# Kernel tuning notes

Hardware: AMD Instinct MI355X
Metric: run time of the kernel (lower is better)

The kernel has to match this reference:

```python
import jax, jax.numpy as jnp
import numpy as np

B, N, D, F = 4, 4096, 1024, 64
LN_EPS = 1e-5
ATTN_EPS = 1e-6


def setup_inputs() -> dict:
    key = jax.random.key(0)
    ks = jax.random.split(key, 9)
    s = 0.02  # small init scale for weights
    return {
        "x": jax.random.normal(ks[0], (B, N, D), dtype=jnp.float32),
        "ln1_w": jnp.ones((D,), jnp.float32),
        "ln1_b": jnp.zeros((D,), jnp.float32),
        "q_w": jax.random.normal(ks[1], (F, D), jnp.float32) * s,
        "q_b": jnp.zeros((F,), jnp.float32),
        "k_w": jax.random.normal(ks[2], (F, D), jnp.float32) * s,
        "k_b": jnp.zeros((F,), jnp.float32),
        "v_w": jax.random.normal(ks[3], (D, D), jnp.float32) * s,
        "v_b": jnp.zeros((D,), jnp.float32),
        "o_w": jax.random.normal(ks[4], (D, D), jnp.float32) * s,
        "o_b": jnp.zeros((D,), jnp.float32),
        "ln2_w": jnp.ones((D,), jnp.float32),
        "ln2_b": jnp.zeros((D,), jnp.float32),
        "f1_w": jax.random.normal(ks[5], (4 * D, D), jnp.float32) * s,
        "f1_b": jnp.zeros((4 * D,), jnp.float32),
        "f2_w": jax.random.normal(ks[6], (D, 4 * D), jnp.float32) * s,
        "f2_b": jnp.zeros((D,), jnp.float32),
    }


def _layer_norm(x, w, b):
    mu = jnp.mean(x, axis=-1, keepdims=True)
    var = jnp.var(x, axis=-1, keepdims=True)
    return (x - mu) * jax.lax.rsqrt(var + LN_EPS) * w + b


def _linear(x, w, b):
    # torch nn.Linear convention: y = x @ w.T + b, w: [out, in]
    return jnp.einsum('bnd,fd->bnf', x, w) + b


def _causal_linear_attn(Q, K, V, eps=ATTN_EPS):
    """Q,K: [B,N,F] positive features; V: [B,N,D]. Recurrent causal scan."""
    b, n, f = K.shape
    d = V.shape[-1]
    Qt = jnp.swapaxes(Q, 0, 1)  # [N,B,F]
    Kt = jnp.swapaxes(K, 0, 1)
    Vt = jnp.swapaxes(V, 0, 1)  # [N,B,D]

    def step(carry, qkv):
        KV, Ks = carry  # [B,F,D], [B,F]
        q, k, v = qkv
        KV = KV + k[:, :, None] * v[:, None, :]
        Ks = Ks + k
        num = jnp.einsum('bf,bfd->bd', q, KV)
        den = jnp.sum(q * Ks, axis=-1, keepdims=True) + eps
        return (KV, Ks), num / den

    init = (jnp.zeros((b, f, d), Q.dtype), jnp.zeros((b, f), Q.dtype))
    _, out = jax.lax.scan(step, init, (Qt, Kt, Vt))
    return jnp.swapaxes(out, 0, 1)  # [B,N,D]


def reference(x, ln1_w, ln1_b, q_w, q_b, k_w, k_b, v_w, v_b,
              o_w, o_b, ln2_w, ln2_b, f1_w, f1_b, f2_w, f2_b):
    x_norm = _layer_norm(x, ln1_w, ln1_b)
    # LinearHopfieldASA, causal=True
    Q = jax.nn.elu(_linear(x_norm, q_w, q_b)) + 1.0  # positive feature map
    K = jax.nn.elu(_linear(x_norm, k_w, k_b)) + 1.0
    V = _linear(x_norm, v_w, v_b)
    attn = _causal_linear_attn(Q, K, V)
    attn = _linear(attn, o_w, o_b)
    x = x + attn
    h = _layer_norm(x, ln2_w, ln2_b)
    h = jax.nn.gelu(_linear(h, f1_w, f1_b), approximate=False)
    x = x + _linear(h, f2_w, f2_b)
    return x
```

## Files before the change

kernel.cpp:

```cpp
#include <hip/hip_runtime.h>
#include <hip/hip_bf16.h>
#include <cstdint>
#include <cstddef>


typedef __attribute__((ext_vector_type(8))) short short8;
typedef __attribute__((ext_vector_type(4))) short short4v;
typedef __attribute__((ext_vector_type(4))) float floatx4;
typedef __attribute__((ext_vector_type(4))) unsigned short ushort4v;

#define DEV static __device__ __forceinline__

DEV float b2f(unsigned short u) {
    union { unsigned int i; float f; } v; v.i = ((unsigned int)u) << 16; return v.f;
}
DEV unsigned short f2b(float f) {
    union { float f; unsigned int i; } v; v.f = f;
    unsigned int i = v.i;
    unsigned int r = (i + 0x7FFFu + ((i >> 16) & 1u)) >> 16;
    return (unsigned short)r;
}

DEV void gl_lds16(const void* g, void* l) {
    __builtin_amdgcn_global_load_lds((const __attribute__((address_space(1))) void*)g,
                                     (__attribute__((address_space(3))) void*)l, 16, 0, 0);
}

__global__ void eel_prep(const float* __restrict__ qw, const float* __restrict__ kw,
                         const float* __restrict__ vw, const float* __restrict__ ow,
                         const float* __restrict__ f1w, const float* __restrict__ f2w,
                         const float* __restrict__ qb, const float* __restrict__ kb,
                         const float* __restrict__ vb,
                         uint16_t* __restrict__ Wqkv, uint16_t* __restrict__ Wo,
                         uint16_t* __restrict__ W1, uint16_t* __restrict__ W2,
                         float* __restrict__ bqkv)
{
    size_t i = (size_t)blockIdx.x * 256 + threadIdx.x;
    size_t stride = (size_t)gridDim.x * 256;
    for (size_t t = i; t < 1152u * 1024u; t += stride) {
        int r = (int)(t >> 10);
        float v = (r < 64) ? qw[t] : (r < 128) ? kw[t - 65536] : vw[t - 131072];
        Wqkv[t] = f2b(v);
    }
    for (size_t t = i; t < 1048576u; t += stride) Wo[t] = f2b(ow[t]);
    for (size_t t = i; t < 4194304u; t += stride) { W1[t] = f2b(f1w[t]); W2[t] = f2b(f2w[t]); }
    if (i < 1152) bqkv[i] = (i < 64) ? qb[i] : (i < 128) ? kb[i - 64] : vb[i - 128];
}

__global__ __launch_bounds__(256) void eel_ln(const float* __restrict__ x,
                                              const float* __restrict__ w,
                                              const float* __restrict__ b,
                                              uint16_t* __restrict__ out)
{
    int row = blockIdx.x, tid = threadIdx.x;
    float4 xv = ((const float4*)(x + (size_t)row * 1024))[tid];
    float s  = xv.x + xv.y + xv.z + xv.w;
    float s2 = xv.x*xv.x + xv.y*xv.y + xv.z*xv.z + xv.w*xv.w;
#pragma unroll
    for (int off = 32; off > 0; off >>= 1) {
        s  += __shfl_down(s, off);
        s2 += __shfl_down(s2, off);
    }
    __shared__ float ps[8];
    int wv = tid >> 6;
    if ((tid & 63) == 0) { ps[wv] = s; ps[4 + wv] = s2; }
    __syncthreads();
    float mu  = (ps[0] + ps[1] + ps[2] + ps[3]) * (1.0f / 1024.0f);
    float var = (ps[4] + ps[5] + ps[6] + ps[7]) * (1.0f / 1024.0f) - mu * mu;
    float rs = rsqrtf(var + 1e-5f);
    float4 wv4 = ((const float4*)w)[tid];
    float4 bv4 = ((const float4*)b)[tid];
    ushort4v o;
    o.x = f2b((xv.x - mu) * rs * wv4.x + bv4.x);
    o.y = f2b((xv.y - mu) * rs * wv4.y + bv4.y);
    o.z = f2b((xv.z - mu) * rs * wv4.z + bv4.z);
    o.w = f2b((xv.w - mu) * rs * wv4.w + bv4.w);
    *(ushort4v*)(out + (size_t)row * 1024 + tid * 4) = o;
}

#define BM 128
#define BN 128
#define BKK 64

__global__ __launch_bounds__(256, 2) void eel_gemm(
    const uint16_t* __restrict__ A, int lda,
    const uint16_t* __restrict__ Bm, int ldb,
    int K,
    const float* __restrict__ bias,
    const float* __restrict__ res,
    uint16_t* __restrict__ outb,
    float* __restrict__ outf,
    int ldc, int mode)
{
    __shared__ uint16_t As[BM * BKK];
    __shared__ uint16_t Bs[BN * BKK];
    int tid = threadIdx.x;
    int lane = tid & 63, w = tid >> 6;
    int lin  = blockIdx.y * gridDim.x + blockIdx.x;
    int span = 8 * gridDim.y;
    int g = lin / span, r = lin % span;
    int bx = g * 8 + (r & 7);
    int by = r >> 3;
    int m0 = bx * BM, n0 = by * BN;
    int wr = (w >> 1) * 64, wc = (w & 1) * 64;
    int quad = lane >> 4, l16 = lane & 15;
    floatx4 acc[4][4] = {};

    int nkb = K / BKK;
    for (int kb = 0; kb < nkb; ++kb) {
        int k0 = kb * BKK;
#pragma unroll
        for (int it = 0; it < 4; ++it) {
            int seg = it * 256 + tid;
            int row = seg >> 3, sub = seg & 7;
            int gs = sub ^ (row & 7);
            gl_lds16(A + (size_t)(m0 + row) * lda + k0 + gs * 8, (char*)As + seg * 16);
            gl_lds16(Bm + (size_t)(n0 + row) * ldb + k0 + gs * 8, (char*)Bs + seg * 16);
        }
        __syncthreads();
#pragma unroll
        for (int ks = 0; ks < 2; ++ks) {
            short8 a[4], b[4];
#pragma unroll
            for (int i = 0; i < 4; i++) {
                int mrow = wr + i * 16 + l16;
                int sa = (ks * 4 + quad) ^ (mrow & 7);
                a[i] = *(const short8*)((const char*)As + mrow * (BKK * 2) + sa * 16);
                int nrow = wc + i * 16 + l16;
                int sb = (ks * 4 + quad) ^ (nrow & 7);
                b[i] = *(const short8*)((const char*)Bs + nrow * (BKK * 2) + sb * 16);
            }
#pragma unroll
            for (int i = 0; i < 4; i++)
#pragma unroll
                for (int j = 0; j < 4; j++)
                    acc[i][j] = __builtin_amdgcn_mfma_f32_16x16x32_bf16(a[i], b[j], acc[i][j], 0, 0, 0);
        }
        __syncthreads();
    }

#pragma unroll
    for (int j = 0; j < 4; j++) {
        int col = n0 + wc + j * 16 + l16;
        float bv = bias ? bias[col] : 0.0f;
#pragma unroll
        for (int i = 0; i < 4; i++) {
#pragma unroll
            for (int r2 = 0; r2 < 4; r2++) {
                int row = m0 + wr + i * 16 + quad * 4 + r2;
                float v = acc[i][j][r2] + bv;
                size_t off = (size_t)row * ldc + col;
                if (mode == 0) {
                    if (col < 128) v = (v > 0.f) ? v + 1.f : __expf(v);
                    outb[off] = f2b(v);
                } else if (mode == 1) {
                    outf[off] = v + res[off];
                } else {
                    float u = 0.7978845608028654f * v * (1.0f + 0.044715f * v * v);
                    float e = __expf(2.0f * u);
                    float t = 1.0f - 2.0f / (e + 1.0f);
                    v = 0.5f * v * (1.0f + t);
                    outb[off] = f2b(v);
                }
            }
        }
    }
}

__global__ __launch_bounds__(256) void eel_attn_s(
    const uint16_t* __restrict__ QKV,
    uint16_t* __restrict__ Sg,
    float* __restrict__ den,
    float* __restrict__ KsA)
{
    int chunk = blockIdx.x, tid = threadIdx.x;
    int tok0 = chunk * 64;
    __shared__ uint16_t Q[64 * 64];
    __shared__ uint16_t Kc[64 * 64];
    __shared__ float denp[64][4];
    {
        int nloc = tid >> 2, seg = tid & 3;
        const uint16_t* src = QKV + (size_t)(tok0 + nloc) * 1152 + seg * 16;
        *(short8*)(Q + nloc * 64 + seg * 16)     = *(const short8*)(src);
        *(short8*)(Q + nloc * 64 + seg * 16 + 8) = *(const short8*)(src + 8);
        src += 64;
        *(short8*)(Kc + nloc * 64 + seg * 16)     = *(const short8*)(src);
        *(short8*)(Kc + nloc * 64 + seg * 16 + 8) = *(const short8*)(src + 8);
    }
    __syncthreads();
    if (tid < 64) {
        float s = 0.f;
        for (int m = 0; m < 64; m++) s += b2f(Kc[m * 64 + tid]);
        KsA[chunk * 64 + tid] = s;
    }
    int n = tid >> 2, mg = tid & 3;
    float dsum = 0.f;
    for (int mi = 0; mi < 16; mi++) {
        int m = mg * 16 + mi;
        size_t soff = (size_t)(tok0 + n) * 64 + m;
        if (m <= n) {
            float s = 0.f;
#pragma unroll
            for (int f = 0; f < 64; f += 8) {
                short8 q8 = *(const short8*)(Q + n * 64 + f);
                short8 k8 = *(const short8*)(Kc + m * 64 + f);
#pragma unroll
                for (int j = 0; j < 8; j++)
                    s += b2f((unsigned short)q8[j]) * b2f((unsigned short)k8[j]);
            }
            dsum += s;
            Sg[soff] = f2b(s);
        } else {
            Sg[soff] = 0;
        }
    }
    denp[n][mg] = dsum;
    __syncthreads();
    if (tid < 64)
        den[tok0 + tid] = denp[tid][0] + denp[tid][1] + denp[tid][2] + denp[tid][3];
}

__global__ __launch_bounds__(256) void eel_attn_kv(
    const uint16_t* __restrict__ QKV,
    uint16_t* __restrict__ KV_A)
{
    int bi = blockIdx.x;
    int chunk = bi >> 3, p = bi & 7;
    int tid = threadIdx.x;
    int tok0 = chunk * 64;
    __shared__ uint16_t Kc[64 * 64];
    __shared__ uint16_t Vp[64 * 128];
    {
        int r = tid >> 2, sg = tid & 3;
        const uint16_t* src = QKV + (size_t)(tok0 + r) * 1152 + 64 + sg * 16;
        *(short8*)(Kc + r * 64 + sg * 16)     = *(const short8*)(src);
        *(short8*)(Kc + r * 64 + sg * 16 + 8) = *(const short8*)(src + 8);
    }
#pragma unroll
    for (int it = 0; it < 2; it++) {
        int s = it * 256 + tid;
        int r = s >> 3, sub = s & 7;
        const uint16_t* src = QKV + (size_t)(tok0 + r) * 1152 + 128 + p * 128 + sub * 16;
        *(short8*)(Vp + r * 128 + sub * 16)     = *(const short8*)(src);
        *(short8*)(Vp + r * 128 + sub * 16 + 8) = *(const short8*)(src + 8);
    }
    __syncthreads();
    int f0 = (tid >> 5) * 8, d0 = (tid & 31) * 4;
    float acc[8][4] = {};
#pragma unroll 2
    for (int m = 0; m < 64; m++) {
        short8 k8 = *(const short8*)(Kc + m * 64 + f0);
        short4v v4 = *(const short4v*)(Vp + m * 128 + d0);
        float v0 = b2f((unsigned short)v4[0]), v1 = b2f((unsigned short)v4[1]);
        float v2 = b2f((unsigned short)v4[2]), v3 = b2f((unsigned short)v4[3]);
#pragma unroll
        for (int i = 0; i < 8; i++) {
            float kk = b2f((unsigned short)k8[i]);
            acc[i][0] += kk * v0; acc[i][1] += kk * v1;
            acc[i][2] += kk * v2; acc[i][3] += kk * v3;
        }
    }
#pragma unroll
    for (int i = 0; i < 8; i++) {
        ushort4v st;
        st.x = f2b(acc[i][0]); st.y = f2b(acc[i][1]);
        st.z = f2b(acc[i][2]); st.w = f2b(acc[i][3]);
        *(ushort4v*)(KV_A + ((size_t)chunk * 64 + f0 + i) * 1024 + p * 128 + d0) = st;
    }
}

__global__ __launch_bounds__(256) void eel_kv_prefix(
    const uint16_t* __restrict__ KV_A, uint16_t* __restrict__ KV_P)
{
    int bi = blockIdx.x;
    int b = bi >> 8, rem = bi & 255;
    int f = rem >> 2;
    int d = (rem & 3) * 256 + threadIdx.x;
    float acc = 0.f;
    for (int cc = 0; cc < 64; cc++) {
        size_t idx = (((size_t)(b * 64 + cc)) * 64 + f) * 1024 + d;
        KV_P[idx] = f2b(acc);
        acc += b2f(KV_A[idx]);
    }
}

__global__ void eel_ks_prefix(const float* __restrict__ KsA, float* __restrict__ KsP)
{
    int b = blockIdx.x, f = threadIdx.x;
    float acc = 0.f;
    for (int cc = 0; cc < 64; cc++) {
        int idx = (b * 64 + cc) * 64 + f;
        KsP[idx] = acc;
        acc += KsA[idx];
    }
}

__global__ __launch_bounds__(256) void eel_attn_out(
    const uint16_t* __restrict__ QKV,
    const uint16_t* __restrict__ Sg,
    const float* __restrict__ den,
    const float* __restrict__ KsP,
    const uint16_t* __restrict__ KV_P,
    uint16_t* __restrict__ attn)
{
    int bi = blockIdx.x;
    int chunk = bi >> 3, p = bi & 7;
    int tid = threadIdx.x;
    int tok0 = chunk * 64;
    __shared__ uint16_t Qt[64 * 64];
    __shared__ uint16_t St[64 * 64];
    __shared__ uint16_t Vp[64 * 128];
    __shared__ uint16_t KVp[64 * 128];
    __shared__ float dfull[64];
    {
        int n = tid >> 2, fs = (tid & 3) * 16;
        const uint16_t* qsrc = QKV + (size_t)(tok0 + n) * 1152 + fs;
        short8 a0 = *(const short8*)(qsrc);
        short8 a1 = *(const short8*)(qsrc + 8);
        const uint16_t* ssrc = Sg + (size_t)(tok0 + n) * 64 + fs;
        short8 s0 = *(const short8*)(ssrc);
        short8 s1 = *(const short8*)(ssrc + 8);
#pragma unroll
        for (int j = 0; j < 8; j++) {
            Qt[(fs + j) * 64 + n]     = (unsigned short)a0[j];
            Qt[(fs + 8 + j) * 64 + n] = (unsigned short)a1[j];
            St[(fs + j) * 64 + n]     = (unsigned short)s0[j];
            St[(fs + 8 + j) * 64 + n] = (unsigned short)s1[j];
        }
    }
#pragma unroll
    for (int it = 0; it < 2; it++) {
        int s = it * 256 + tid;
        int r = s >> 3, sub = s & 7;
        const uint16_t* vsrc = QKV + (size_t)(tok0 + r) * 1152 + 128 + p * 128 + sub * 16;
        *(short8*)(Vp + r * 128 + sub * 16)     = *(const short8*)(vsrc);
        *(short8*)(Vp + r * 128 + sub * 16 + 8) = *(const short8*)(vsrc + 8);
        const uint16_t* kvsrc = KV_P + ((size_t)(chunk * 64 + r)) * 1024 + p * 128 + sub * 16;
        *(short8*)(KVp + r * 128 + sub * 16)     = *(const short8*)(kvsrc);
        *(short8*)(KVp + r * 128 + sub * 16 + 8) = *(const short8*)(kvsrc + 8);
    }
    __syncthreads();
    if (tid < 64) {
        float s = 0.f;
        for (int f = 0; f < 64; f++)
            s += b2f(Qt[f * 64 + tid]) * KsP[chunk * 64 + f];
        dfull[tid] = s + den[tok0 + tid] + 1e-6f;
    }
    __syncthreads();
    int n0 = (tid >> 5) * 8, d0 = (tid & 31) * 4;
    float acc[8][4] = {};
#pragma unroll 2
    for (int f = 0; f < 64; f++) {
        short8 q8 = *(const short8*)(Qt + f * 64 + n0);
        short4v kv4 = *(const short4v*)(KVp + f * 128 + d0);
        float v0 = b2f((unsigned short)kv4[0]), v1 = b2f((unsigned short)kv4[1]);
        float v2 = b2f((unsigned short)kv4[2]), v3 = b2f((unsigned short)kv4[3]);
#pragma unroll
        for (int i = 0; i < 8; i++) {
            float q = b2f((unsigned short)q8[i]);
            acc[i][0] += q * v0; acc[i][1] += q * v1;
            acc[i][2] += q * v2; acc[i][3] += q * v3;
        }
    }
#pragma unroll 2
    for (int m = 0; m < 64; m++) {
        short8 s8 = *(const short8*)(St + m * 64 + n0);
        short4v v4 = *(const short4v*)(Vp + m * 128 + d0);
        float v0 = b2f((unsigned short)v4[0]), v1 = b2f((unsigned short)v4[1]);
        float v2 = b2f((unsigned short)v4[2]), v3 = b2f((unsigned short)v4[3]);
#pragma unroll
        for (int i = 0; i < 8; i++) {
            float q = b2f((unsigned short)s8[i]);
            acc[i][0] += q * v0; acc[i][1] += q * v1;
            acc[i][2] += q * v2; acc[i][3] += q * v3;
        }
    }
#pragma unroll
    for (int i = 0; i < 8; i++) {
        int n = n0 + i;
        float rinv = 1.0f / dfull[n];
        ushort4v st;
        st.x = f2b(acc[i][0] * rinv);
        st.y = f2b(acc[i][1] * rinv);
        st.z = f2b(acc[i][2] * rinv);
        st.w = f2b(acc[i][3] * rinv);
        *(ushort4v*)(attn + (size_t)(tok0 + n) * 1024 + p * 128 + d0) = st;
    }
}

extern "C" void kernel_launch(void* const* d_in, const int* in_sizes, int n_in,
                              void* d_out, int out_size, void* d_ws, size_t ws_size,
                              hipStream_t stream)
{
    (void)in_sizes; (void)n_in; (void)out_size; (void)ws_size;
    const float* x     = (const float*)d_in[0];
    const float* ln1w  = (const float*)d_in[1];
    const float* ln1b  = (const float*)d_in[2];
    const float* qw    = (const float*)d_in[3];
    const float* qb    = (const float*)d_in[4];
    const float* kw    = (const float*)d_in[5];
    const float* kb    = (const float*)d_in[6];
    const float* vw    = (const float*)d_in[7];
    const float* vb    = (const float*)d_in[8];
    const float* ow    = (const float*)d_in[9];
    const float* ob    = (const float*)d_in[10];
    const float* ln2w  = (const float*)d_in[11];
    const float* ln2b  = (const float*)d_in[12];
    const float* f1w   = (const float*)d_in[13];
    const float* f1b   = (const float*)d_in[14];
    const float* f2w   = (const float*)d_in[15];
    const float* f2bs  = (const float*)d_in[16];
    float* out = (float*)d_out;
    char* ws = (char*)d_ws;

    const size_t o_Wqkv = 0;
    const size_t o_Wo   = o_Wqkv + 2359296;
    const size_t o_W1   = o_Wo   + 2097152;
    const size_t o_W2   = o_W1   + 8388608;
    const size_t o_bqkv = o_W2   + 8388608;
    const size_t O_XN   = 21238272;
    const size_t O_QKV  = 54792704;
    const size_t O_S    = 92541440;
    const size_t O_DEN  = 94638592;
    const size_t O_KSA  = 94704128;
    const size_t O_KSP  = 94769664;
    const size_t O_KVA  = 94835200;
    const size_t O_KVP  = 161944064;

    uint16_t* Wqkv  = (uint16_t*)(ws + o_Wqkv);
    uint16_t* Wo    = (uint16_t*)(ws + o_Wo);
    uint16_t* W1    = (uint16_t*)(ws + o_W1);
    uint16_t* W2    = (uint16_t*)(ws + o_W2);
    float*    bqkv  = (float*)(ws + o_bqkv);
    uint16_t* xn    = (uint16_t*)(ws + O_XN);
    uint16_t* attn  = (uint16_t*)(ws + O_XN);
    uint16_t* QKV   = (uint16_t*)(ws + O_QKV);
    uint16_t* hnorm = (uint16_t*)(ws + O_QKV);
    uint16_t* Sg    = (uint16_t*)(ws + O_S);
    float*    den   = (float*)(ws + O_DEN);
    float*    KsA   = (float*)(ws + O_KSA);
    float*    KsP   = (float*)(ws + O_KSP);
    uint16_t* KV_A  = (uint16_t*)(ws + O_KVA);
    uint16_t* hbuf  = (uint16_t*)(ws + O_KVA);
    uint16_t* KV_P  = (uint16_t*)(ws + O_KVP);

    eel_prep<<<4096, 256, 0, stream>>>(qw, kw, vw, ow, f1w, f2w, qb, kb, vb,
                                       Wqkv, Wo, W1, W2, bqkv);
    eel_ln<<<16384, 256, 0, stream>>>(x, ln1w, ln1b, xn);
    eel_gemm<<<dim3(128, 9), 256, 0, stream>>>(xn, 1024, Wqkv, 1024, 1024,
                                               bqkv, nullptr, QKV, nullptr, 1152, 0);
    eel_attn_s<<<256, 256, 0, stream>>>(QKV, Sg, den, KsA);
    eel_attn_kv<<<2048, 256, 0, stream>>>(QKV, KV_A);
    eel_kv_prefix<<<1024, 256, 0, stream>>>(KV_A, KV_P);
    eel_ks_prefix<<<4, 64, 0, stream>>>(KsA, KsP);
    eel_attn_out<<<2048, 256, 0, stream>>>(QKV, Sg, den, KsP, KV_P, attn);
    eel_gemm<<<dim3(128, 8), 256, 0, stream>>>(attn, 1024, Wo, 1024, 1024,
                                               ob, x, nullptr, out, 1024, 1);
    eel_ln<<<16384, 256, 0, stream>>>(out, ln2w, ln2b, hnorm);
    for (int strip = 0; strip < 2; strip++) {
        size_t noff = (size_t)strip * 2048;
        eel_gemm<<<dim3(128, 16), 256, 0, stream>>>(hnorm, 1024, W1 + noff * 1024, 1024, 1024,
                                                    f1b + noff, nullptr, hbuf, nullptr, 2048, 2);
        eel_gemm<<<dim3(128, 8), 256, 0, stream>>>(hbuf, 2048, W2 + noff, 4096, 2048,
                                                   strip == 0 ? f2bs : nullptr, out, nullptr,
                                                   out, 1024, 1);
    }
}
```

Baseline: 857.8 us.

## Replace GEMM with 256x256-tile, 4-stage pipelined 8-wave kernel

Replaces the 128x128 single-buffered GEMM with a 256x256-tile kernel using 512 threads, a 4-deep LDS ring of BK=32 stages filled by direct global-to-LDS loads, explicit vmcnt waits, split-phase MFMA with setprio, and a new XOR swizzle. It also changes the tile rasterization and adds bounds clamping for the 1152-wide QKV output. The aim is to overlap global loads with MFMA work and raise data reuse per block. In exchange it uses more LDS and registers (32 accumulators per wave) and launches fewer blocks, which can leave CUs underused on the smaller GEMMs.

```diff
diff --git a/kernel.cpp b/kernel.cpp
--- a/kernel.cpp
+++ b/kernel.cpp
@@ -78,93 +78,162 @@
     *(ushort4v*)(out + (size_t)row * 1024 + tid * 4) = o;
 }
 
-#define BM 128
-#define BN 128
-#define BKK 64
-
-__global__ __launch_bounds__(256, 2) void eel_gemm(
+__global__ __launch_bounds__(512, 2) void eel_gemm256(
     const uint16_t* __restrict__ A, int lda,
-    const uint16_t* __restrict__ Bm, int ldb,
+    const uint16_t* __restrict__ Bm, int ldb, int bmax,
     int K,
     const float* __restrict__ bias,
     const float* __restrict__ res,
-    uint16_t* __restrict__ outb,
-    float* __restrict__ outf,
-    int ldc, int mode)
-{
-    __shared__ uint16_t As[BM * BKK];
-    __shared__ uint16_t Bs[BN * BKK];
+    uint16_t* __restrict__ outb, float* __restrict__ outf,
+    int ldc, int mode, int nvalid)
+{
+    __shared__ uint16_t sA[4][8192];
+    __shared__ uint16_t sB[4][8192];
     int tid = threadIdx.x;
     int lane = tid & 63, w = tid >> 6;
-    int lin  = blockIdx.y * gridDim.x + blockIdx.x;
-    int span = 8 * gridDim.y;
-    int g = lin / span, r = lin % span;
-    int bx = g * 8 + (r & 7);
-    int by = r >> 3;
-    int m0 = bx * BM, n0 = by * BN;
-    int wr = (w >> 1) * 64, wc = (w & 1) * 64;
     int quad = lane >> 4, l16 = lane & 15;
-    floatx4 acc[4][4] = {};
-
-    int nkb = K / BKK;
-    for (int kb = 0; kb < nkb; ++kb) {
-        int k0 = kb * BKK;
-#pragma unroll
-        for (int it = 0; it < 4; ++it) {
-            int seg = it * 256 + tid;
-            int row = seg >> 3, sub = seg & 7;
-            int gs = sub ^ (row & 7);
-            gl_lds16(A + (size_t)(m0 + row) * lda + k0 + gs * 8, (char*)As + seg * 16);
-            gl_lds16(Bm + (size_t)(n0 + row) * ldb + k0 + gs * 8, (char*)Bs + seg * 16);
-        }
-        __syncthreads();
-#pragma unroll
-        for (int ks = 0; ks < 2; ++ks) {
-            short8 a[4], b[4];
-#pragma unroll
-            for (int i = 0; i < 4; i++) {
-                int mrow = wr + i * 16 + l16;
-                int sa = (ks * 4 + quad) ^ (mrow & 7);
-                a[i] = *(const short8*)((const char*)As + mrow * (BKK * 2) + sa * 16);
-                int nrow = wc + i * 16 + l16;
-                int sb = (ks * 4 + quad) ^ (nrow & 7);
-                b[i] = *(const short8*)((const char*)Bs + nrow * (BKK * 2) + sb * 16);
-            }
-#pragma unroll
-            for (int i = 0; i < 4; i++)
-#pragma unroll
-                for (int j = 0; j < 4; j++)
-                    acc[i][j] = __builtin_amdgcn_mfma_f32_16x16x32_bf16(a[i], b[j], acc[i][j], 0, 0, 0);
-        }
-        __syncthreads();
-    }
+
+    int nblk = gridDim.x, qch = nblk >> 3;
+    int lin  = blockIdx.x;
+    int tile = (lin & 7) * qch + (lin >> 3);
+    int bx = tile & 63, by = tile >> 6;
+    int m0 = bx << 8, n0 = by << 8;
+
+    int wr = (w >> 2) * 128;
+    int wc = (w & 3) * 64;
+    int rA = wr + l16;
+    int rB = wc + l16;
+
+    floatx4 acc[8][4] = {};
+    short8 a0, a1, a2, a3, b0, b1, b2, b3;
+
+    int srow = tid >> 2, sseg = tid & 3;
+    int sgs  = sseg ^ ((srow >> 1) & 3);
+    const uint16_t* aptr0 = A + (size_t)(m0 + srow) * lda + sgs * 8;
+    const uint16_t* aptr1 = A + (size_t)(m0 + srow + 128) * lda + sgs * 8;
+    int br0 = n0 + srow;       if (br0 >= bmax) br0 = 0;
+    int br1 = n0 + srow + 128; if (br1 >= bmax) br1 = 0;
+    const uint16_t* bptr0 = Bm + (size_t)br0 * ldb + sgs * 8;
+    const uint16_t* bptr1 = Bm + (size_t)br1 * ldb + sgs * 8;
+
+#define STAGE_A(Tn) do {                                                      \
+    gl_lds16(aptr0 + (Tn) * 32, (char*)sA[(Tn) & 3] + tid * 16);              \
+    gl_lds16(aptr1 + (Tn) * 32, (char*)sA[(Tn) & 3] + 8192 + tid * 16);       \
+} while (0)
+#define STAGE_B(Tn) do {                                                      \
+    gl_lds16(bptr0 + (Tn) * 32, (char*)sB[(Tn) & 3] + tid * 16);              \
+    gl_lds16(bptr1 + (Tn) * 32, (char*)sB[(Tn) & 3] + 8192 + tid * 16);       \
+} while (0)
+#define NOSTG do { } while (0)
+#define FRG(buf, r) (*(const short8*)((const char*)(buf) + (size_t)(r) * 64 + \
+                     ((quad ^ (((r) >> 1) & 3)) * 16)))
+#define VMW8 do { asm volatile("s_waitcnt vmcnt(8)"); __builtin_amdgcn_sched_barrier(0); } while (0)
+#define VMW4 do { asm volatile("s_waitcnt vmcnt(4)"); __builtin_amdgcn_sched_barrier(0); } while (0)
+#define VMW0 do { asm volatile("s_waitcnt vmcnt(0)"); __builtin_amdgcn_sched_barrier(0); } while (0)
+#define MFMA16(bb) do {                                                                        \
+    acc[(bb)+0][0]=__builtin_amdgcn_mfma_f32_16x16x32_bf16(a0,b0,acc[(bb)+0][0],0,0,0);        \
+    acc[(bb)+0][1]=__builtin_amdgcn_mfma_f32_16x16x32_bf16(a0,b1,acc[(bb)+0][1],0,0,0);        \
+    acc[(bb)+0][2]=__builtin_amdgcn_mfma_f32_16x16x32_bf16(a0,b2,acc[(bb)+0][2],0,0,0);        \
+    acc[(bb)+0][3]=__builtin_amdgcn_mfma_f32_16x16x32_bf16(a0,b3,acc[(bb)+0][3],0,0,0);        \
+    acc[(bb)+1][0]=__builtin_amdgcn_mfma_f32_16x16x32_bf16(a1,b0,acc[(bb)+1][0],0,0,0);        \
+    acc[(bb)+1][1]=__builtin_amdgcn_mfma_f32_16x16x32_bf16(a1,b1,acc[(bb)+1][1],0,0,0);        \
+    acc[(bb)+1][2]=__builtin_amdgcn_mfma_f32_16x16x32_bf16(a1,b2,acc[(bb)+1][2],0,0,0);        \
+    acc[(bb)+1][3]=__builtin_amdgcn_mfma_f32_16x16x32_bf16(a1,b3,acc[(bb)+1][3],0,0,0);        \
+    acc[(bb)+2][0]=__builtin_amdgcn_mfma_f32_16x16x32_bf16(a2,b0,acc[(bb)+2][0],0,0,0);        \
+    acc[(bb)+2][1]=__builtin_amdgcn_mfma_f32_16x16x32_bf16(a2,b1,acc[(bb)+2][1],0,0,0);        \
+    acc[(bb)+2][2]=__builtin_amdgcn_mfma_f32_16x16x32_bf16(a2,b2,acc[(bb)+2][2],0,0,0);        \
+    acc[(bb)+2][3]=__builtin_amdgcn_mfma_f32_16x16x32_bf16(a2,b3,acc[(bb)+2][3],0,0,0);        \
+    acc[(bb)+3][0]=__builtin_amdgcn_mfma_f32_16x16x32_bf16(a3,b0,acc[(bb)+3][0],0,0,0);        \
+    acc[(bb)+3][1]=__builtin_amdgcn_mfma_f32_16x16x32_bf16(a3,b1,acc[(bb)+3][1],0,0,0);        \
+    acc[(bb)+3][2]=__builtin_amdgcn_mfma_f32_16x16x32_bf16(a3,b2,acc[(bb)+3][2],0,0,0);        \
+    acc[(bb)+3][3]=__builtin_amdgcn_mfma_f32_16x16x32_bf16(a3,b3,acc[(bb)+3][3],0,0,0);        \
+} while (0)
+#define PHASE1(bi, STG) do {                                                  \
+    const uint16_t* Ab_ = sA[bi]; const uint16_t* Bb_ = sB[bi];               \
+    a0 = FRG(Ab_, rA +  0); a1 = FRG(Ab_, rA + 16);                           \
+    a2 = FRG(Ab_, rA + 32); a3 = FRG(Ab_, rA + 48);                           \
+    b0 = FRG(Bb_, rB +  0); b1 = FRG(Bb_, rB + 16);                           \
+    b2 = FRG(Bb_, rB + 32); b3 = FRG(Bb_, rB + 48);                           \
+    STG;                                                                      \
+    __builtin_amdgcn_s_barrier();                                             \
+    asm volatile("s_waitcnt lgkmcnt(0)");                                     \
+    __builtin_amdgcn_sched_barrier(0);                                        \
+    __builtin_amdgcn_s_setprio(1);                                            \
+    MFMA16(0);                                                                \
+    __builtin_amdgcn_s_setprio(0);                                            \
+    __builtin_amdgcn_s_barrier();                                             \
+} while (0)
+#define PHASE2(bi, STG, VM) do {                                              \
+    const uint16_t* Ab_ = sA[bi];                                             \
+    a0 = FRG(Ab_, rA + 64); a1 = FRG(Ab_, rA + 80);                           \
+    a2 = FRG(Ab_, rA + 96); a3 = FRG(Ab_, rA + 112);                          \
+    STG;                                                                      \
+    __builtin_amdgcn_s_barrier();                                             \
+    asm volatile("s_waitcnt lgkmcnt(0)");                                     \
+    __builtin_amdgcn_sched_barrier(0);                                        \
+    __builtin_amdgcn_s_setprio(1);                                            \
+    MFMA16(4);                                                                \
+    __builtin_amdgcn_s_setprio(0);                                            \
+    VM;                                                                       \
+    __builtin_amdgcn_s_barrier();                                             \
+} while (0)
+
+    STAGE_A(0); STAGE_B(0);
+    STAGE_A(1); STAGE_B(1);
+    STAGE_A(2); STAGE_B(2);
+    asm volatile("s_waitcnt vmcnt(8)");
+    __builtin_amdgcn_sched_barrier(0);
+    __builtin_amdgcn_s_barrier();
+
+    int nT = K >> 5;
+    int T = 0;
+    for (; T < nT - 3; ++T) {
+        int bi = T & 3;
+        PHASE1(bi, STAGE_A(T + 3));
+        PHASE2(bi, STAGE_B(T + 3), VMW8);
+    }
+    PHASE1(T & 3, NOSTG); PHASE2(T & 3, NOSTG, VMW4); ++T;
+    PHASE1(T & 3, NOSTG); PHASE2(T & 3, NOSTG, VMW0); ++T;
+    PHASE1(T & 3, NOSTG); PHASE2(T & 3, NOSTG, NOSTG);
 
 #pragma unroll
     for (int j = 0; j < 4; j++) {
         int col = n0 + wc + j * 16 + l16;
-        float bv = bias ? bias[col] : 0.0f;
-#pragma unroll
-        for (int i = 0; i < 4; i++) {
-#pragma unroll
-            for (int r2 = 0; r2 < 4; r2++) {
-                int row = m0 + wr + i * 16 + quad * 4 + r2;
-                float v = acc[i][j][r2] + bv;
-                size_t off = (size_t)row * ldc + col;
-                if (mode == 0) {
-                    if (col < 128) v = (v > 0.f) ? v + 1.f : __expf(v);
-                    outb[off] = f2b(v);
-                } else if (mode == 1) {
-                    outf[off] = v + res[off];
-                } else {
-                    float u = 0.7978845608028654f * v * (1.0f + 0.044715f * v * v);
-                    float e = __expf(2.0f * u);
-                    float t = 1.0f - 2.0f / (e + 1.0f);
-                    v = 0.5f * v * (1.0f + t);
-                    outb[off] = f2b(v);
+        if (col < nvalid) {
+            float bv = bias ? bias[col] : 0.0f;
+#pragma unroll
+            for (int i = 0; i < 8; i++) {
+#pragma unroll
+                for (int r2 = 0; r2 < 4; r2++) {
+                    int row = m0 + wr + i * 16 + quad * 4 + r2;
+                    float v = acc[i][j][r2] + bv;
+                    size_t off = (size_t)row * ldc + col;
+                    if (mode == 0) {
+                        if (col < 128) v = (v > 0.f) ? v + 1.f : __expf(v);
+                        outb[off] = f2b(v);
+                    } else if (mode == 1) {
+                        outf[off] = v + res[off];
+                    } else {
+                        float u = 0.7978845608028654f * v * (1.0f + 0.044715f * v * v);
+                        float e = __expf(2.0f * u);
+                        float t = 1.0f - 2.0f / (e + 1.0f);
+                        v = 0.5f * v * (1.0f + t);
+                        outb[off] = f2b(v);
+                    }
                 }
             }
         }
     }
+#undef STAGE_A
+#undef STAGE_B
+#undef NOSTG
+#undef FRG
+#undef VMW8
+#undef VMW4
+#undef VMW0
+#undef MFMA16
+#undef PHASE1
+#undef PHASE2
 }
 
 __global__ __launch_bounds__(256) void eel_attn_s(
@@ -447,22 +516,23 @@
     eel_prep<<<4096, 256, 0, stream>>>(qw, kw, vw, ow, f1w, f2w, qb, kb, vb,
                                        Wqkv, Wo, W1, W2, bqkv);
     eel_ln<<<16384, 256, 0, stream>>>(x, ln1w, ln1b, xn);
-    eel_gemm<<<dim3(128, 9), 256, 0, stream>>>(xn, 1024, Wqkv, 1024, 1024,
-                                               bqkv, nullptr, QKV, nullptr, 1152, 0);
+    eel_gemm256<<<320, 512, 0, stream>>>(xn, 1024, Wqkv, 1024, 1152, 1024,
+                                         bqkv, nullptr, QKV, nullptr, 1152, 0, 1152);
     eel_attn_s<<<256, 256, 0, stream>>>(QKV, Sg, den, KsA);
     eel_attn_kv<<<2048, 256, 0, stream>>>(QKV, KV_A);
     eel_kv_prefix<<<1024, 256, 0, stream>>>(KV_A, KV_P);
     eel_ks_prefix<<<4, 64, 0, stream>>>(KsA, KsP);
     eel_attn_out<<<2048, 256, 0, stream>>>(QKV, Sg, den, KsP, KV_P, attn);
-    eel_gemm<<<dim3(128, 8), 256, 0, stream>>>(attn, 1024, Wo, 1024, 1024,
-                                               ob, x, nullptr, out, 1024, 1);
+    eel_gemm256<<<256, 512, 0, stream>>>(attn, 1024, Wo, 1024, 1024, 1024,
+                                         ob, x, nullptr, out, 1024, 1, 1024);
     eel_ln<<<16384, 256, 0, stream>>>(out, ln2w, ln2b, hnorm);
     for (int strip = 0; strip < 2; strip++) {
         size_t noff = (size_t)strip * 2048;
-        eel_gemm<<<dim3(128, 16), 256, 0, stream>>>(hnorm, 1024, W1 + noff * 1024, 1024, 1024,
-                                                    f1b + noff, nullptr, hbuf, nullptr, 2048, 2);
-        eel_gemm<<<dim3(128, 8), 256, 0, stream>>>(hbuf, 2048, W2 + noff, 4096, 2048,
-                                                   strip == 0 ? f2bs : nullptr, out, nullptr,
-                                                   out, 1024, 1);
-    }
-}
+        eel_gemm256<<<512, 512, 0, stream>>>(hnorm, 1024, W1 + noff * 1024, 1024, 2048,
+                                             1024, f1b + noff, nullptr, hbuf, nullptr,
+                                             2048, 2, 2048);
+        eel_gemm256<<<256, 512, 0, stream>>>(hbuf, 2048, W2 + noff, 4096, 1024,
+                                             2048, strip == 0 ? f2bs : nullptr, out,
+                                             nullptr, out, 1024, 1, 1024);
+    }
+}
```

New measurement: 1.120 ms. 1.31x slower.
